# Kernel tuning notes

Hardware: AMD Instinct MI355X
Metric: run time of the kernel (lower is better)

The kernel has to match this reference:

```python
import jax, jax.numpy as jnp
import numpy as np

N, F, O = 8192, 1024, 1024
NUM_NEIGH = 10


def setup_inputs() -> dict:
    key = jax.random.key(0)
    k1, k2, k3, k4, k5 = jax.random.split(key, 5)
    X = jax.random.normal(k1, (N, F), dtype=jnp.float32)
    A = jax.random.uniform(k2, (N, N), dtype=jnp.float32)
    stdv = 1.0 / np.sqrt(O)
    W = jax.random.uniform(k3, (2 * F, O), dtype=jnp.float32, minval=-stdv, maxval=stdv)
    b = jax.random.uniform(k4, (O,), dtype=jnp.float32, minval=-stdv, maxval=stdv)
    # Uniform neighbor sampling (original uses np.random.choice over range(N) per node)
    sampled_idx = jax.random.randint(k5, (N, NUM_NEIGH), 0, N, dtype=jnp.int32)
    return {"X": X, "A": A, "W": W, "b": b, "sampled_idx": sampled_idx}


def reference(X, A, W, b, sampled_idx):
    # aggregate: mean of uniformly sampled neighbor features per node.
    # (The matrix_power of the normalized A in the original is dead code; A's
    #  values never influence the output.)
    gathered = X[sampled_idx]                 # [N, num_neigh, F]
    aggregated = jnp.mean(gathered, axis=1)   # [N, F]
    combined = jnp.concatenate([X, aggregated], axis=1)  # [N, 2F]
    return combined @ W + b                   # [N, O]
```

## Files before the change

kernel.cpp:

```cpp
#include <hip/hip_runtime.h>
#include <stdint.h>

#define NN 8192
#define FD 1024
#define OD 1024
#define KD 2048
#define NB 10

typedef short bf16x8 __attribute__((ext_vector_type(8)));
typedef float f32x4  __attribute__((ext_vector_type(4)));

static __device__ __forceinline__ float bf2f(ushort u) {
  union { uint32_t i; float f; } v; v.i = ((uint32_t)u) << 16; return v.f;
}
static __device__ __forceinline__ ushort f2bf(float f) {
  union { float f; uint32_t i; } v; v.f = f;
  uint32_t x = v.i;
  return (ushort)((x + 0x7FFFu + ((x >> 16) & 1u)) >> 16);
}
static __device__ __forceinline__ bf16x8 cvt8(const float* p) {
  const float4 a = *reinterpret_cast<const float4*>(p);
  const float4 b = *reinterpret_cast<const float4*>(p + 4);
  bf16x8 v;
  v[0] = (short)f2bf(a.x); v[1] = (short)f2bf(a.y);
  v[2] = (short)f2bf(a.z); v[3] = (short)f2bf(a.w);
  v[4] = (short)f2bf(b.x); v[5] = (short)f2bf(b.y);
  v[6] = (short)f2bf(b.z); v[7] = (short)f2bf(b.w);
  return v;
}

static __device__ __forceinline__ void async16(const ushort* g, ushort* l) {
  __builtin_amdgcn_global_load_lds(
      (const __attribute__((address_space(1))) uint32_t*)(const void*)g,
      (__attribute__((address_space(3))) uint32_t*)(void*)l, 16, 0, 0);
}

__global__ __launch_bounds__(256) void xconv(const float* __restrict__ X,
                                             ushort* __restrict__ Ab) {
  const int q   = blockIdx.x * 256 + threadIdx.x;
  const int row = q >> 7;
  const int col = (q & 127) * 8;
  const bf16x8 v = cvt8(X + (size_t)row * FD + col);
  *reinterpret_cast<bf16x8*>(Ab + (size_t)row * KD + col) = v;
}

__global__ __launch_bounds__(256) void aggk(const int* __restrict__ idx,
                                            ushort* __restrict__ Ab) {
  const int row  = blockIdx.x * 2 + (threadIdx.x >> 7);
  const int lane = threadIdx.x & 127;
  const int col  = lane * 8;
  const int* ip = idx + (size_t)row * NB;
  int nb[NB];
#pragma unroll
  for (int j = 0; j < NB; ++j) nb[j] = ip[j];
  float acc[8] = {0.f, 0.f, 0.f, 0.f, 0.f, 0.f, 0.f, 0.f};
#pragma unroll
  for (int j = 0; j < NB; ++j) {
    const uint4 v = *reinterpret_cast<const uint4*>(Ab + (size_t)nb[j] * KD + col);
    const ushort* u = reinterpret_cast<const ushort*>(&v);
#pragma unroll
    for (int e = 0; e < 8; ++e) acc[e] += bf2f(u[e]);
  }
  bf16x8 o;
#pragma unroll
  for (int e = 0; e < 8; ++e) o[e] = (short)f2bf(acc[e] * 0.1f);
  *reinterpret_cast<bf16x8*>(Ab + (size_t)row * KD + FD + col) = o;
}

__global__ __launch_bounds__(1024) void wconv(const float* __restrict__ W,
                                              ushort* __restrict__ Wtb) {
  __shared__ float tile[64][65];
  const int k0 = blockIdx.x * 64;
  const int n0 = blockIdx.y * 64;
  const int tx = threadIdx.x;
  const int ty = threadIdx.y;
#pragma unroll
  for (int r = 0; r < 4; ++r) {
    const int kl = ty + r * 16;
    tile[kl][tx] = W[(size_t)(k0 + kl) * OD + n0 + tx];
  }
  __syncthreads();
#pragma unroll
  for (int r = 0; r < 4; ++r) {
    const int nl = ty + r * 16;
    Wtb[(size_t)(n0 + nl) * KD + k0 + tx] = f2bf(tile[tx][nl]);
  }
}

__global__ __launch_bounds__(512, 2) void gemm_256x128(const ushort* __restrict__ Ab,
                                                       const ushort* __restrict__ Wtb,
                                                       const float* __restrict__ Bias,
                                                       float* __restrict__ Out) {
  __shared__ ushort lA[3 * 256 * 64];
  __shared__ ushort lB[3 * 128 * 64];
  const int t  = threadIdx.x;
  const int id  = blockIdx.x;
  const int xcd = id & 7;
  const int j   = id >> 3;
  const int m0  = (xcd * 4 + (j >> 3)) * 256;
  const int n0  = (j & 7) * 128;

  const int wave = t >> 6;
  const int lane = t & 63;
  const int wm   = (wave >> 1) * 64;
  const int wn   = (wave & 1) * 64;
  const int l15  = lane & 15;
  const int quad = lane >> 4;

  f32x4 acc[4][4];
#pragma unroll
  for (int i = 0; i < 4; ++i)
#pragma unroll
    for (int jj = 0; jj < 4; ++jj) acc[i][jj] = (f32x4){0.f, 0.f, 0.f, 0.f};

  const ushort* gA[4];
  const ushort* gB[2];
#pragma unroll
  for (int i = 0; i < 4; ++i) {
    const int q   = i * 512 + t;
    const int row = q >> 3;
    const int c   = ((q & 7) - row) & 7;
    gA[i] = Ab + (size_t)(m0 + row) * KD + c * 8;
  }
#pragma unroll
  for (int i = 0; i < 2; ++i) {
    const int q   = i * 512 + t;
    const int row = q >> 3;
    const int c   = ((q & 7) - row) & 7;
    gB[i] = Wtb + (size_t)(n0 + row) * KD + c * 8;
  }

  auto STAGE = [&](int tile, int buf) {
    const int k0 = tile * 64;
    ushort* la = lA + buf * (256 * 64);
    ushort* lb = lB + buf * (128 * 64);
#pragma unroll
    for (int i = 0; i < 4; ++i) async16(gA[i] + k0, la + (i * 512 + t) * 8);
#pragma unroll
    for (int i = 0; i < 2; ++i) async16(gB[i] + k0, lb + (i * 512 + t) * 8);
  };

  auto COMPUTE = [&](int buf) {
    const ushort* la = lA + buf * (256 * 64);
    const ushort* lb = lB + buf * (128 * 64);
#pragma unroll
    for (int s = 0; s < 2; ++s) {
      const int c = s * 4 + quad;
      bf16x8 afr[4], bfr[4];
#pragma unroll
      for (int mi = 0; mi < 4; ++mi) {
        const int r = wm + mi * 16 + l15;
        afr[mi] = *reinterpret_cast<const bf16x8*>(la + r * 64 + ((c + r) & 7) * 8);
      }
#pragma unroll
      for (int ni = 0; ni < 4; ++ni) {
        const int r = wn + ni * 16 + l15;
        bfr[ni] = *reinterpret_cast<const bf16x8*>(lb + r * 64 + ((c + r) & 7) * 8);
      }
      __builtin_amdgcn_s_setprio(1);
#pragma unroll
      for (int mi = 0; mi < 4; ++mi)
#pragma unroll
        for (int ni = 0; ni < 4; ++ni)
          acc[mi][ni] = __builtin_amdgcn_mfma_f32_16x16x32_bf16(afr[mi], bfr[ni], acc[mi][ni], 0, 0, 0);
      __builtin_amdgcn_s_setprio(0);
    }
  };

  STAGE(0, 0); STAGE(1, 1); STAGE(2, 2);

  int buf = 0;
  for (int tile = 0; tile <= 28; ++tile) {
    asm volatile("s_waitcnt vmcnt(12)\ns_barrier" ::: "memory");
    COMPUTE(buf);
    asm volatile("s_barrier" ::: "memory");
    STAGE(tile + 3, buf);
    buf = (buf == 2) ? 0 : buf + 1;
  }
  asm volatile("s_waitcnt vmcnt(12)\ns_barrier" ::: "memory");
  COMPUTE(buf);
  buf = (buf == 2) ? 0 : buf + 1;
  asm volatile("s_waitcnt vmcnt(6)\ns_barrier" ::: "memory");
  COMPUTE(buf);
  buf = (buf == 2) ? 0 : buf + 1;
  asm volatile("s_waitcnt vmcnt(0)\ns_barrier" ::: "memory");
  COMPUTE(buf);

#pragma unroll
  for (int ni = 0; ni < 4; ++ni) {
    const int gn = n0 + wn + ni * 16 + l15;
    const float bv = Bias[gn];
#pragma unroll
    for (int mi = 0; mi < 4; ++mi) {
      const int gm = m0 + wm + mi * 16 + quad * 4;
#pragma unroll
      for (int r = 0; r < 4; ++r)
        Out[(size_t)(gm + r) * OD + gn] = acc[mi][ni][r] + bv;
    }
  }
}

__global__ __launch_bounds__(256) void gemm_fused(const float* __restrict__ X,
                                                  const float* __restrict__ W,
                                                  const float* __restrict__ Bias,
                                                  const int* __restrict__ idx,
                                                  float* __restrict__ Out) {
  __shared__ ushort lA[128 * 32];
  __shared__ ushort lB[32 * 128];
  const int t    = threadIdx.x;
  const int m0   = blockIdx.y * 128;
  const int n0   = blockIdx.x * 128;
  const int wave = t >> 6;
  const int lane = t & 63;
  const int wm   = (wave & 1) * 64;
  const int wn   = (wave >> 1) * 64;
  const int l15  = lane & 15;
  const int quad = lane >> 4;

  f32x4 acc[4][4];
#pragma unroll
  for (int i = 0; i < 4; ++i)
#pragma unroll
    for (int j = 0; j < 4; ++j) acc[i][j] = (f32x4){0.f, 0.f, 0.f, 0.f};

  for (int kt = 0; kt < KD / 32; ++kt) {
    const int k0 = kt * 32;
    if (k0 < FD) {
#pragma unroll
      for (int r = 0; r < 2; ++r) {
        const int q = r * 256 + t;
        const int row = q >> 2, ch = q & 3;
        *reinterpret_cast<bf16x8*>(lA + q * 8) =
            cvt8(X + (size_t)(m0 + row) * FD + k0 + ch * 8);
      }
    } else {
      const int kc = k0 - FD;
#pragma unroll
      for (int r = 0; r < 2; ++r) {
        const int q = r * 256 + t;
        const int row = q >> 2, ch = q & 3;
        float a8[8] = {0.f, 0.f, 0.f, 0.f, 0.f, 0.f, 0.f, 0.f};
        const int* ip = idx + (size_t)(m0 + row) * NB;
#pragma unroll
        for (int j = 0; j < NB; ++j) {
          const float* p = X + (size_t)ip[j] * FD + kc + ch * 8;
          const float4 a = *(const float4*)p;
          const float4 b = *(const float4*)(p + 4);
          a8[0] += a.x; a8[1] += a.y; a8[2] += a.z; a8[3] += a.w;
          a8[4] += b.x; a8[5] += b.y; a8[6] += b.z; a8[7] += b.w;
        }
        bf16x8 v;
#pragma unroll
        for (int e = 0; e < 8; ++e) v[e] = (short)f2bf(a8[e] * 0.1f);
        *reinterpret_cast<bf16x8*>(lA + q * 8) = v;
      }
    }
#pragma unroll
    for (int r = 0; r < 2; ++r) {
      const int q = r * 256 + t;
      const int kr = q >> 4, ch = q & 15;
      *reinterpret_cast<bf16x8*>(lB + q * 8) =
          cvt8(W + (size_t)(k0 + kr) * OD + n0 + ch * 8);
    }
    __syncthreads();

    bf16x8 afr[4], bfr[4];
#pragma unroll
    for (int mi = 0; mi < 4; ++mi)
      afr[mi] = *reinterpret_cast<const bf16x8*>(lA + (wm + mi * 16 + l15) * 32 + quad * 8);
#pragma unroll
    for (int ni = 0; ni < 4; ++ni) {
      const int col = wn + ni * 16 + l15;
#pragma unroll
      for (int j = 0; j < 8; ++j)
        bfr[ni][j] = (short)lB[(quad * 8 + j) * 128 + col];
    }
#pragma unroll
    for (int mi = 0; mi < 4; ++mi)
#pragma unroll
      for (int ni = 0; ni < 4; ++ni)
        acc[mi][ni] = __builtin_amdgcn_mfma_f32_16x16x32_bf16(afr[mi], bfr[ni], acc[mi][ni], 0, 0, 0);
    __syncthreads();
  }
#pragma unroll
  for (int ni = 0; ni < 4; ++ni) {
    const int gn = n0 + wn + ni * 16 + l15;
    const float bv = Bias[gn];
#pragma unroll
    for (int mi = 0; mi < 4; ++mi) {
      const int gm = m0 + wm + mi * 16 + quad * 4;
#pragma unroll
      for (int r = 0; r < 4; ++r)
        Out[(size_t)(gm + r) * OD + gn] = acc[mi][ni][r] + bv;
    }
  }
}

extern "C" void kernel_launch(void* const* d_in, const int* in_sizes, int n_in,
                              void* d_out, int out_size, void* d_ws, size_t ws_size,
                              hipStream_t stream) {
  const float* X   = (const float*)d_in[0];
  const float* W   = (const float*)d_in[2];
  const float* b   = (const float*)d_in[3];
  const int*   idx = (const int*)d_in[4];
  float* out = (float*)d_out;

  const size_t need = ((size_t)NN * KD + (size_t)OD * KD) * sizeof(ushort);
  if (ws_size >= need) {
    ushort* Ab  = (ushort*)d_ws;
    ushort* Wtb = Ab + (size_t)NN * KD;

    xconv<<<NN * FD / (256 * 8), 256, 0, stream>>>(X, Ab);
    wconv<<<dim3(KD / 64, OD / 64), dim3(64, 16), 0, stream>>>(W, Wtb);
    aggk<<<NN / 2, 256, 0, stream>>>(idx, Ab);
    gemm_256x128<<<256, 512, 0, stream>>>(Ab, Wtb, b, out);
  } else {
    gemm_fused<<<dim3(OD / 128, NN / 128), 256, 0, stream>>>(X, W, b, idx, out);
  }
}
```

Baseline: 396.9 us.

## Restructure GEMM main loop into interleaved phases with split A/B prefetch

Rewrites the bf16 MFMA GEMM main loop so each k-tile runs as two half-k phases. The global-to-LDS copy for tile+2 is split, with A issued during the first phase and B during the second, and barriers placed around each MFMA cluster. LDS fragment offsets are precomputed once outside the loop, and the prefetch distance drops from three tiles ahead to two. The aim is finer interleaving of memory issue with MFMA work and less address arithmetic, at the cost of more barriers per tile and a shallower prefetch.

```diff
diff --git a/kernel.cpp b/kernel.cpp
--- a/kernel.cpp
+++ b/kernel.cpp
@@ -87,10 +87,10 @@
   }
 }
 
-__global__ __launch_bounds__(512, 2) void gemm_256x128(const ushort* __restrict__ Ab,
-                                                       const ushort* __restrict__ Wtb,
-                                                       const float* __restrict__ Bias,
-                                                       float* __restrict__ Out) {
+__global__ __launch_bounds__(512, 2) void gemm_8ph(const ushort* __restrict__ Ab,
+                                                   const ushort* __restrict__ Wtb,
+                                                   const float* __restrict__ Bias,
+                                                   float* __restrict__ Out) {
   __shared__ ushort lA[3 * 256 * 64];
   __shared__ ushort lB[3 * 128 * 64];
   const int t  = threadIdx.x;
@@ -130,33 +130,58 @@
     gB[i] = Wtb + (size_t)(n0 + row) * KD + c * 8;
   }
 
-  auto STAGE = [&](int tile, int buf) {
-    const int k0 = tile * 64;
-    ushort* la = lA + buf * (256 * 64);
-    ushort* lb = lB + buf * (128 * 64);
-#pragma unroll
-    for (int i = 0; i < 4; ++i) async16(gA[i] + k0, la + (i * 512 + t) * 8);
-#pragma unroll
-    for (int i = 0; i < 2; ++i) async16(gB[i] + k0, lb + (i * 512 + t) * 8);
-  };
-
-  auto COMPUTE = [&](int buf) {
-    const ushort* la = lA + buf * (256 * 64);
-    const ushort* lb = lB + buf * (128 * 64);
-#pragma unroll
-    for (int s = 0; s < 2; ++s) {
-      const int c = s * 4 + quad;
+  int offA[2][4], offB[2][4];
+#pragma unroll
+  for (int s = 0; s < 2; ++s) {
+    const int c = s * 4 + quad;
+#pragma unroll
+    for (int mi = 0; mi < 4; ++mi) {
+      const int r = wm + mi * 16 + l15;
+      offA[s][mi] = r * 64 + ((c + r) & 7) * 8;
+    }
+#pragma unroll
+    for (int ni = 0; ni < 4; ++ni) {
+      const int r = wn + ni * 16 + l15;
+      offB[s][ni] = r * 64 + ((c + r) & 7) * 8;
+    }
+  }
+
+  {
+    ushort* la0 = lA;            ushort* lb0 = lB;
+    ushort* la1 = lA + 256 * 64; ushort* lb1 = lB + 128 * 64;
+#pragma unroll
+    for (int i = 0; i < 4; ++i) async16(gA[i], la0 + (i * 512 + t) * 8);
+#pragma unroll
+    for (int i = 0; i < 2; ++i) async16(gB[i], lb0 + (i * 512 + t) * 8);
+#pragma unroll
+    for (int i = 0; i < 4; ++i) async16(gA[i] + 64, la1 + (i * 512 + t) * 8);
+#pragma unroll
+    for (int i = 0; i < 2; ++i) async16(gB[i] + 64, lb1 + (i * 512 + t) * 8);
+  }
+  asm volatile("s_waitcnt vmcnt(6)\ns_barrier" ::: "memory");
+
+  int cur = 0, nx2 = 2;
+  for (int tile = 0; tile < 32; ++tile) {
+    const ushort* la = lA + cur * (256 * 64);
+    const ushort* lb = lB + cur * (128 * 64);
+    ushort* sa = lA + nx2 * (256 * 64);
+    ushort* sb = lB + nx2 * (128 * 64);
+    const bool st = tile < 30;
+    const int k2 = (tile + 2) * 64;
+
+    {
       bf16x8 afr[4], bfr[4];
 #pragma unroll
-      for (int mi = 0; mi < 4; ++mi) {
-        const int r = wm + mi * 16 + l15;
-        afr[mi] = *reinterpret_cast<const bf16x8*>(la + r * 64 + ((c + r) & 7) * 8);
+      for (int mi = 0; mi < 4; ++mi)
+        afr[mi] = *reinterpret_cast<const bf16x8*>(la + offA[0][mi]);
+#pragma unroll
+      for (int ni = 0; ni < 4; ++ni)
+        bfr[ni] = *reinterpret_cast<const bf16x8*>(lb + offB[0][ni]);
+      if (st) {
+#pragma unroll
+        for (int i = 0; i < 4; ++i) async16(gA[i] + k2, sa + (i * 512 + t) * 8);
       }
-#pragma unroll
-      for (int ni = 0; ni < 4; ++ni) {
-        const int r = wn + ni * 16 + l15;
-        bfr[ni] = *reinterpret_cast<const bf16x8*>(lb + r * 64 + ((c + r) & 7) * 8);
-      }
+      asm volatile("s_barrier" ::: "memory");
       __builtin_amdgcn_s_setprio(1);
 #pragma unroll
       for (int mi = 0; mi < 4; ++mi)
@@ -164,27 +189,38 @@
         for (int ni = 0; ni < 4; ++ni)
           acc[mi][ni] = __builtin_amdgcn_mfma_f32_16x16x32_bf16(afr[mi], bfr[ni], acc[mi][ni], 0, 0, 0);
       __builtin_amdgcn_s_setprio(0);
-    }
-  };
-
-  STAGE(0, 0); STAGE(1, 1); STAGE(2, 2);
-
-  int buf = 0;
-  for (int tile = 0; tile <= 28; ++tile) {
-    asm volatile("s_waitcnt vmcnt(12)\ns_barrier" ::: "memory");
-    COMPUTE(buf);
-    asm volatile("s_barrier" ::: "memory");
-    STAGE(tile + 3, buf);
-    buf = (buf == 2) ? 0 : buf + 1;
-  }
-  asm volatile("s_waitcnt vmcnt(12)\ns_barrier" ::: "memory");
-  COMPUTE(buf);
-  buf = (buf == 2) ? 0 : buf + 1;
-  asm volatile("s_waitcnt vmcnt(6)\ns_barrier" ::: "memory");
-  COMPUTE(buf);
-  buf = (buf == 2) ? 0 : buf + 1;
-  asm volatile("s_waitcnt vmcnt(0)\ns_barrier" ::: "memory");
-  COMPUTE(buf);
+      asm volatile("s_barrier" ::: "memory");
+    }
+    {
+      bf16x8 afr[4], bfr[4];
+#pragma unroll
+      for (int mi = 0; mi < 4; ++mi)
+        afr[mi] = *reinterpret_cast<const bf16x8*>(la + offA[1][mi]);
+#pragma unroll
+      for (int ni = 0; ni < 4; ++ni)
+        bfr[ni] = *reinterpret_cast<const bf16x8*>(lb + offB[1][ni]);
+      if (st) {
+#pragma unroll
+        for (int i = 0; i < 2; ++i) async16(gB[i] + k2, sb + (i * 512 + t) * 8);
+      }
+      asm volatile("s_barrier" ::: "memory");
+      __builtin_amdgcn_s_setprio(1);
+#pragma unroll
+      for (int mi = 0; mi < 4; ++mi)
+#pragma unroll
+        for (int ni = 0; ni < 4; ++ni)
+          acc[mi][ni] = __builtin_amdgcn_mfma_f32_16x16x32_bf16(afr[mi], bfr[ni], acc[mi][ni], 0, 0, 0);
+      __builtin_amdgcn_s_setprio(0);
+      asm volatile("s_barrier" ::: "memory");
+    }
+    if (tile < 30) {
+      asm volatile("s_waitcnt vmcnt(6)\ns_barrier" ::: "memory");
+    } else if (tile == 30) {
+      asm volatile("s_waitcnt vmcnt(0)\ns_barrier" ::: "memory");
+    }
+    cur = (cur == 2) ? 0 : cur + 1;
+    nx2 = (nx2 == 2) ? 0 : nx2 + 1;
+  }
 
 #pragma unroll
   for (int ni = 0; ni < 4; ++ni) {
@@ -313,7 +349,7 @@
     xconv<<<NN * FD / (256 * 8), 256, 0, stream>>>(X, Ab);
     wconv<<<dim3(KD / 64, OD / 64), dim3(64, 16), 0, stream>>>(W, Wtb);
     aggk<<<NN / 2, 256, 0, stream>>>(idx, Ab);
-    gemm_256x128<<<256, 512, 0, stream>>>(Ab, Wtb, b, out);
+    gemm_8ph<<<256, 512, 0, stream>>>(Ab, Wtb, b, out);
   } else {
     gemm_fused<<<dim3(OD / 128, NN / 128), 256, 0, stream>>>(X, W, b, idx, out);
   }
```

Result: faster. 388.4 us (-2.2%).
